# Performance work log

Measured on AMD Instinct MI355X. Metric: run time of the kernel, lower is better.

The kernel has to match this reference:

```python
import jax, jax.numpy as jnp
import numpy as np

CS = 128            # config.chunk_size
K = 8               # config.k + 1
EPS = 1e-6          # config.eps
L = K * CS          # extended_len = 1024


def setup_inputs() -> dict:
    key = jax.random.key(0)
    k1, k2 = jax.random.split(key)
    B, T, E = 2, 8192, 256
    x = jax.random.normal(k1, (B, T, E), dtype=jnp.float32)
    # xavier_normal_ on [CS, L]: std = sqrt(2 / (fan_in + fan_out))
    std = np.sqrt(2.0 / (CS + L)).astype(np.float32)
    down_proj = jax.random.normal(k2, (CS, L), dtype=jnp.float32) * std
    return {"x": x, "down_proj": down_proj}


def reference(x, down_proj):
    B, T, E = x.shape
    N = T // CS  # T chosen divisible by CS, so the pad branch is a no-op
    chunks = x.reshape(B, N, CS, E)

    # --- per-chunk retrieval scores (vectorized over the causal chunk loop) ---
    cn = chunks / (jnp.linalg.norm(chunks, axis=-1, keepdims=True) + EPS)
    # row-wise cosine sims between every pair of chunks: [B,N,N,CS,CS]
    sims = jnp.einsum('bice,bjde->bijcd', cn, cn)
    scores = sims.max(axis=-1).sum(axis=-1)              # [B,N,N]
    i_idx = jnp.arange(N)
    causal = i_idx[None, :] < i_idx[:, None]             # j < i allowed
    NEG = jnp.asarray(-1e9, x.dtype)
    scores = jnp.where(causal[None], scores, NEG)

    # --- topk selection, weights (num_sel_i = min(i, K-1)) ---
    vals, idx = jax.lax.top_k(scores, K - 1)             # descending, [B,N,K-1]
    num_sel = jnp.minimum(i_idx, K - 1)                  # [N]
    vmin_slot = jnp.clip(num_sel - 1, 0, K - 2)          # last valid slot = min of topk vals
    v_min = jnp.take_along_axis(vals, jnp.broadcast_to(vmin_slot[None, :, None], (B, N, 1)), axis=-1)
    slot = jnp.arange(K - 1)
    valid = slot[None, :] < num_sel[:, None]             # [N,K-1]
    w = jnp.where(valid[None], vals / (v_min + EPS), 0.0)  # [B,N,K-1]

    # --- weighted gather of selected chunks ---
    b_idx = jnp.arange(B)[:, None, None]
    sel = chunks[b_idx, idx]                             # [B,N,K-1,CS,E]
    weighted = sel * w[..., None, None]

    # --- left-pad to L: zeros occupy leftmost slots, then topk-ordered chunks, then cur ---
    shift = jnp.maximum(0, (K - 1) - i_idx)              # [N]
    src = jnp.clip(slot[None, :] - shift[:, None], 0, K - 2)   # [N,K-1]
    n_idx = jnp.arange(N)[None, :, None]
    arranged = weighted[b_idx, n_idx, src[None]]         # [B,N,K-1,CS,E]
    keep = slot[None, :] >= shift[:, None]
    arranged = jnp.where(keep[None, :, :, None, None], arranged, 0.0)

    ext = jnp.concatenate([arranged.reshape(B, N, (K - 1) * CS, E), chunks], axis=2)  # [B,N,L,E]
    # down_proj @ ext + x_chunks, then contract back to [B,T,E]
    out = jnp.einsum('cl,bnle->bnce', down_proj, ext) + chunks
    return out.reshape(B, N * CS, E)
```

## Files before the change

kernel.cpp:

```cpp
#include <hip/hip_runtime.h>
#include <hip/hip_bf16.h>

#define CS     128
#define EDIM   256
#define NBATCH 2
#define TLEN   8192
#define NCHUNK 64
#define LEXT   1024
#define KSEL   7

typedef __attribute__((ext_vector_type(8))) short   short8;
typedef __attribute__((ext_vector_type(4))) float   floatx4;

__device__ inline short bf16_of(float f) {
    __hip_bfloat16 h = __float2bfloat16(f);
    return *(short*)&h;
}
__device__ inline float f_of_bf16(short s) {
    __hip_bfloat16 h = *(__hip_bfloat16*)&s;
    return __bfloat162float(h);
}

__device__ inline void gl_lds16(const void* g, void* l) {
    __builtin_amdgcn_global_load_lds(
        (const __attribute__((address_space(1))) unsigned int*)g,
        (__attribute__((address_space(3))) unsigned int*)l, 16, 0, 0);
}

__global__ __launch_bounds__(256) void prep_kernel(const float* __restrict__ x,
                                                   const float* __restrict__ dp,
                                                   short* __restrict__ cn_hi,
                                                   short* __restrict__ cn_lo,
                                                   short* __restrict__ xt_hi,
                                                   short* __restrict__ dp_hi) {
    const int bx = blockIdx.x;
    if (bx >= 256) {
        int t = (bx - 256) * 256 + threadIdx.x;
#pragma unroll
        for (int u = 0; u < 16; ++u) {
            int idx = (t * 16 + u) * 4;
            float4 v = *(const float4*)(dp + idx);
            *(short4*)(dp_hi + idx) =
                make_short4(bf16_of(v.x), bf16_of(v.y), bf16_of(v.z), bf16_of(v.w));
        }
        return;
    }

    __shared__ float tile[64 * 257];
    const int b = bx >> 7, t0 = (bx & 127) * 64;
    const int tid = threadIdx.x;
    const int r = tid >> 2, q = tid & 3;

    const float* src = x + ((size_t)(b * TLEN + t0 + r)) * EDIM + q * 64;
    float* trow = &tile[r * 257 + q * 64];
    float s = 0.f;
#pragma unroll
    for (int u = 0; u < 16; ++u) {
        float4 v = *(const float4*)(src + u * 4);
        s += v.x * v.x + v.y * v.y + v.z * v.z + v.w * v.w;
        trow[u * 4 + 0] = v.x; trow[u * 4 + 1] = v.y;
        trow[u * 4 + 2] = v.z; trow[u * 4 + 3] = v.w;
    }
    s += __shfl_xor(s, 1);
    s += __shfl_xor(s, 2);
    const float rn = 1.0f / (sqrtf(s) + 1e-6f);

    short* ch = cn_hi + ((size_t)(b * TLEN + t0 + r)) * EDIM + q * 64;
    short* cl = cn_lo + ((size_t)(b * TLEN + t0 + r)) * EDIM + q * 64;
#pragma unroll
    for (int u = 0; u < 16; ++u) {
        short hs[4], ls[4];
#pragma unroll
        for (int k2 = 0; k2 < 4; ++k2) {
            float c = trow[u * 4 + k2] * rn;
            hs[k2] = bf16_of(c);
            ls[k2] = bf16_of(c - f_of_bf16(hs[k2]));
        }
        *(short4*)(ch + u * 4) = make_short4(hs[0], hs[1], hs[2], hs[3]);
        *(short4*)(cl + u * 4) = make_short4(ls[0], ls[1], ls[2], ls[3]);
    }
    __syncthreads();

    const int g16 = tid >> 4, tq = tid & 15;
#pragma unroll
    for (int it = 0; it < 16; ++it) {
        int e = g16 + it * 16;
        short hs2[4];
#pragma unroll
        for (int g = 0; g < 4; ++g)
            hs2[g] = bf16_of(tile[(tq * 4 + g) * 257 + e]);
        *(short4*)(xt_hi + ((size_t)(b * EDIM + e)) * TLEN + t0 + tq * 4)
            = make_short4(hs2[0], hs2[1], hs2[2], hs2[3]);
    }
}

__global__ __launch_bounds__(256) void scores_mfma(const short* __restrict__ cn_hi,
                                                   const short* __restrict__ cn_lo,
                                                   float* __restrict__ scores) {
    __shared__ short tiles[4][4096];
    double* red2  = (double*)&tiles[0][0];
    float*  redbuf = (float*)&tiles[0][8];

    const int p = blockIdx.x, b = blockIdx.y;
    int i = (int)((1.0f + sqrtf(1.0f + 8.0f * (float)p)) * 0.5f);
    while (i * (i - 1) / 2 > p) --i;
    while (i * (i + 1) / 2 <= p) ++i;
    const int j = p - i * (i - 1) / 2;

    const int tid  = threadIdx.x;
    const int w    = tid >> 6, lane = tid & 63;
    const int wr   = w >> 1, wc = w & 1;
    const int quad = lane >> 4, l15 = lane & 15;

    const short* sarr  = (w & 1) ? cn_lo : cn_hi;
    const size_t sbase = ((size_t)b * TLEN + ((w >> 1) ? j : i) * CS) * EDIM;
    const int rr  = lane >> 2;
    const int c16 = (lane & 3) * 8;
    const int csw = c16 ^ (((rr >> 1) & 3) * 8);
    const int q8  = (quad ^ ((l15 >> 1) & 3)) * 8;

    floatx4 acc[4][4];
#pragma unroll
    for (int rt = 0; rt < 4; ++rt)
#pragma unroll
        for (int ct = 0; ct < 4; ++ct) acc[rt][ct] = (floatx4){0.f, 0.f, 0.f, 0.f};

    for (int ks = 0; ks < 8; ++ks) {
        const short* gsrc = sarr + sbase + ks * 32 + csw;
        short* ldst = &tiles[w][0];
#pragma unroll
        for (int t = 0; t < 8; ++t)
            gl_lds16(gsrc + (size_t)(16 * t + rr) * EDIM, ldst + t * 512);
        __syncthreads();

        short8 bh[4], bl[4];
#pragma unroll
        for (int ct = 0; ct < 4; ++ct) {
            int r = wc * 64 + ct * 16 + l15;
            bh[ct] = *(const short8*)&tiles[2][r * 32 + q8];
            bl[ct] = *(const short8*)&tiles[3][r * 32 + q8];
        }
#pragma unroll
        for (int rt = 0; rt < 4; ++rt) {
            int r = wr * 64 + rt * 16 + l15;
            short8 ah = *(const short8*)&tiles[0][r * 32 + q8];
            short8 al = *(const short8*)&tiles[1][r * 32 + q8];
#pragma unroll
            for (int ct = 0; ct < 4; ++ct) {
                acc[rt][ct] = __builtin_amdgcn_mfma_f32_16x16x32_bf16(ah, bh[ct], acc[rt][ct], 0, 0, 0);
                acc[rt][ct] = __builtin_amdgcn_mfma_f32_16x16x32_bf16(ah, bl[ct], acc[rt][ct], 0, 0, 0);
                acc[rt][ct] = __builtin_amdgcn_mfma_f32_16x16x32_bf16(al, bh[ct], acc[rt][ct], 0, 0, 0);
            }
        }
        __syncthreads();
    }

#pragma unroll
    for (int rt = 0; rt < 4; ++rt) {
        float m[4];
#pragma unroll
        for (int reg = 0; reg < 4; ++reg) {
            float mm = acc[rt][0][reg];
#pragma unroll
            for (int ct = 1; ct < 4; ++ct) mm = fmaxf(mm, acc[rt][ct][reg]);
            m[reg] = mm;
        }
#pragma unroll
        for (int off = 1; off < 16; off <<= 1)
#pragma unroll
            for (int reg = 0; reg < 4; ++reg) m[reg] = fmaxf(m[reg], __shfl_xor(m[reg], off));
        if (l15 == 0) {
#pragma unroll
            for (int reg = 0; reg < 4; ++reg)
                redbuf[wc * 128 + wr * 64 + rt * 16 + quad * 4 + reg] = m[reg];
        }
    }
    __syncthreads();

    double part = 0.0;
    if (tid < 128) part = (double)fmaxf(redbuf[tid], redbuf[128 + tid]);
#pragma unroll
    for (int off = 1; off < 64; off <<= 1) part += __shfl_xor(part, off);
    if (lane == 0 && w < 2) red2[w] = part;
    __syncthreads();
    if (tid == 0) scores[(b * NCHUNK + i) * NCHUNK + j] = (float)(red2[0] + red2[1]);
}

__global__ __launch_bounds__(256) void out_mfma(const float* __restrict__ x,
                                                const short* __restrict__ dph,
                                                const short* __restrict__ xth,
                                                const float* __restrict__ scores,
                                                float* __restrict__ out) {
    __shared__ short As[2][128 * 32];
    __shared__ short Bs[2][64 * 32];
    __shared__ int   slist[8], sslot[8], snum;
    __shared__ float swei[8];

    const int eq = blockIdx.x, n = blockIdx.y, b = blockIdx.z;
    const int e0 = eq * 64;
    const int tid  = threadIdx.x;
    const int w    = tid >> 6, lane = tid & 63;
    const int wr   = w >> 1, wc = w & 1;
    const int quad = lane >> 4, l15 = lane & 15;
    const int rr   = lane >> 2;
    const int c16  = (lane & 3) * 8;
    const int csw  = c16 ^ (((rr >> 1) & 3) * 8);
    const int q8   = (quad ^ ((l15 >> 1) & 3)) * 8;

    if (w == 0) {
        const float* srow = scores + (b * NCHUNK + n) * NCHUNK;
        const int nsel = n < KSEL ? n : KSEL;
        float v = (lane < n) ? srow[lane] : -3.0e38f;
        float vals[KSEL];
        int   idxs[KSEL];
        for (int s2 = 0; s2 < nsel; ++s2) {
            float bv = v; int bi = lane;
#pragma unroll
            for (int off = 1; off < 64; off <<= 1) {
                float ov = __shfl_xor(bv, off);
                int   oi = __shfl_xor(bi, off);
                if (ov > bv || (ov == bv && oi < bi)) { bv = ov; bi = oi; }
            }
            vals[s2] = bv; idxs[s2] = bi;
            if (lane == bi) v = -3.0e38f;
        }
        if (lane == 0) {
            float vmin = (nsel > 0) ? vals[nsel - 1] : 0.0f;
            float inv  = 1.0f / (vmin + 1e-6f);
            int shift  = KSEL - nsel;
            int c = 0;
            for (int s2 = 0; s2 < 8; ++s2) {
                int jj; float ww;
                if (s2 < KSEL) {
                    int tt = s2 - shift;
                    if (tt >= 0) { jj = idxs[tt]; ww = vals[tt] * inv; }
                    else         { jj = -1;       ww = 0.0f; }
                } else { jj = n; ww = 1.0f; }
                if (jj >= 0) { slist[c] = jj; sslot[c] = s2; swei[c] = ww; ++c; }
            }
            snum = c;
        }
    }
    __syncthreads();
    const int NS = snum * 4;

    auto stage = [&](int st, int bf) {
        int sv = st >> 2, kk = st & 3;
        if (w < 2) {
            const short* gsrc = dph + (size_t)(sslot[sv] * 128 + kk * 32) + csw;
#pragma unroll
            for (int t = 0; t < 4; ++t)
                gl_lds16(gsrc + (size_t)(w * 64 + t * 16 + rr) * LEXT,
                         &As[bf][(w * 64 + t * 16) * 32]);
        } else {
            const short* gsrc = xth + ((size_t)(b * EDIM + e0)) * TLEN
                                + (size_t)(slist[sv] * CS + kk * 32) + csw;
#pragma unroll
            for (int t = 0; t < 2; ++t)
                gl_lds16(gsrc + (size_t)((w - 2) * 32 + t * 16 + rr) * TLEN,
                         &Bs[bf][((w - 2) * 32 + t * 16) * 32]);
        }
    };

    floatx4 accT[4][2], accP[4][2];
#pragma unroll
    for (int rt = 0; rt < 4; ++rt)
#pragma unroll
        for (int ct = 0; ct < 2; ++ct) accT[rt][ct] = (floatx4){0.f, 0.f, 0.f, 0.f};

    stage(0, 0);
    __syncthreads();

    int buf = 0;
    for (int st = 0; st < NS; ++st) {
        if (st + 1 < NS) stage(st + 1, buf ^ 1);

        if ((st & 3) == 0) {
#pragma unroll
            for (int rt = 0; rt < 4; ++rt)
#pragma unroll
                for (int ct = 0; ct < 2; ++ct) accP[rt][ct] = (floatx4){0.f, 0.f, 0.f, 0.f};
        }

        short8 bh[2];
#pragma unroll
        for (int ct = 0; ct < 2; ++ct) {
            int e = wc * 32 + ct * 16 + l15;
            bh[ct] = *(const short8*)&Bs[buf][e * 32 + q8];
        }
#pragma unroll
        for (int rt = 0; rt < 4; ++rt) {
            int r = wr * 64 + rt * 16 + l15;
            short8 ah = *(const short8*)&As[buf][r * 32 + q8];
#pragma unroll
            for (int ct = 0; ct < 2; ++ct)
                accP[rt][ct] = __builtin_amdgcn_mfma_f32_16x16x32_bf16(ah, bh[ct], accP[rt][ct], 0, 0, 0);
        }

        if ((st & 3) == 3) {
            float wcur = swei[st >> 2];
#pragma unroll
            for (int rt = 0; rt < 4; ++rt)
#pragma unroll
                for (int ct = 0; ct < 2; ++ct)
#pragma unroll
                    for (int reg = 0; reg < 4; ++reg)
                        accT[rt][ct][reg] += wcur * accP[rt][ct][reg];
        }
        __syncthreads();
        buf ^= 1;
    }

#pragma unroll
    for (int rt = 0; rt < 4; ++rt)
#pragma unroll
        for (int ct = 0; ct < 2; ++ct) {
#pragma unroll
            for (int reg = 0; reg < 4; ++reg) {
                int row = wr * 64 + rt * 16 + quad * 4 + reg;
                int col = wc * 32 + ct * 16 + l15;
                size_t o = ((size_t)(b * TLEN + n * CS + row)) * EDIM + e0 + col;
                out[o] = accT[rt][ct][reg] + x[o];
            }
        }
}

extern "C" void kernel_launch(void* const* d_in, const int* in_sizes, int n_in,
                              void* d_out, int out_size, void* d_ws, size_t ws_size,
                              hipStream_t stream) {
    const float* x  = (const float*)d_in[0];
    const float* dp = (const float*)d_in[1];
    float* out = (float*)d_out;

    char* ws = (char*)d_ws;
    short* cn_hi  = (short*)(ws);
    short* cn_lo  = (short*)(ws + (8u << 20));
    short* xt_hi  = (short*)(ws + (16u << 20));
    short* dp_hi  = (short*)(ws + (24u << 20));
    float* scores = (float*)(ws + (25u << 20));

    prep_kernel <<<dim3(264), 256, 0, stream>>>(x, dp, cn_hi, cn_lo, xt_hi, dp_hi);
    scores_mfma <<<dim3(NCHUNK * (NCHUNK - 1) / 2, NBATCH), 256, 0, stream>>>(cn_hi, cn_lo, scores);
    out_mfma    <<<dim3(4, NCHUNK, NBATCH), 256, 0, stream>>>(x, dp_hi, xt_hi, scores, out);
}
```

Before: 213.7 us.

## Double-buffer scores kernel and use partial vmcnt waits with raw barriers

The scores kernel now double-buffers its LDS tiles and prefetches the next k-slice before computing on the current one. Both the scores and projection kernels replace __syncthreads with a raw s_barrier preceded by a partial s_waitcnt vmcnt, so prefetch loads stay in flight across the barrier. MFMA sections are wrapped in s_setprio to favour matrix issue. The aim is to overlap global-to-LDS loads with MFMA work. The cost is double the LDS in the scores kernel, which may lower occupancy, and a risk of races if the hand-written vmcnt counts are wrong.

```diff
diff --git a/kernel.cpp b/kernel.cpp
--- a/kernel.cpp
+++ b/kernel.cpp
@@ -26,6 +26,8 @@
         (const __attribute__((address_space(1))) unsigned int*)g,
         (__attribute__((address_space(3))) unsigned int*)l, 16, 0, 0);
 }
+
+#define RAW_BAR() asm volatile("s_barrier" ::: "memory")
 
 __global__ __launch_bounds__(256) void prep_kernel(const float* __restrict__ x,
                                                    const float* __restrict__ dp,
@@ -97,9 +99,9 @@
 __global__ __launch_bounds__(256) void scores_mfma(const short* __restrict__ cn_hi,
                                                    const short* __restrict__ cn_lo,
                                                    float* __restrict__ scores) {
-    __shared__ short tiles[4][4096];
-    double* red2  = (double*)&tiles[0][0];
-    float*  redbuf = (float*)&tiles[0][8];
+    __shared__ short tiles[2][4][4096];
+    double* red2   = (double*)&tiles[0][0][0];
+    float*  redbuf = (float*)&tiles[0][0][8];
 
     const int p = blockIdx.x, b = blockIdx.y;
     int i = (int)((1.0f + sqrtf(1.0f + 8.0f * (float)p)) * 0.5f);
@@ -119,32 +121,44 @@
     const int csw = c16 ^ (((rr >> 1) & 3) * 8);
     const int q8  = (quad ^ ((l15 >> 1) & 3)) * 8;
 
-    floatx4 acc[4][4];
-#pragma unroll
-    for (int rt = 0; rt < 4; ++rt)
-#pragma unroll
-        for (int ct = 0; ct < 4; ++ct) acc[rt][ct] = (floatx4){0.f, 0.f, 0.f, 0.f};
-
-    for (int ks = 0; ks < 8; ++ks) {
+    auto stage = [&](int ks, int bf) {
         const short* gsrc = sarr + sbase + ks * 32 + csw;
-        short* ldst = &tiles[w][0];
+        short* ldst = &tiles[bf][w][0];
 #pragma unroll
         for (int t = 0; t < 8; ++t)
             gl_lds16(gsrc + (size_t)(16 * t + rr) * EDIM, ldst + t * 512);
-        __syncthreads();
+    };
+
+    floatx4 acc[4][4];
+#pragma unroll
+    for (int rt = 0; rt < 4; ++rt)
+#pragma unroll
+        for (int ct = 0; ct < 4; ++ct) acc[rt][ct] = (floatx4){0.f, 0.f, 0.f, 0.f};
+
+    stage(0, 0);
+    int buf = 0;
+    for (int ks = 0; ks < 8; ++ks) {
+        if (ks < 7) {
+            stage(ks + 1, buf ^ 1);
+            asm volatile("s_waitcnt vmcnt(8)" ::: "memory");
+        } else {
+            asm volatile("s_waitcnt vmcnt(0)" ::: "memory");
+        }
+        RAW_BAR();
 
         short8 bh[4], bl[4];
 #pragma unroll
         for (int ct = 0; ct < 4; ++ct) {
             int r = wc * 64 + ct * 16 + l15;
-            bh[ct] = *(const short8*)&tiles[2][r * 32 + q8];
-            bl[ct] = *(const short8*)&tiles[3][r * 32 + q8];
-        }
+            bh[ct] = *(const short8*)&tiles[buf][2][r * 32 + q8];
+            bl[ct] = *(const short8*)&tiles[buf][3][r * 32 + q8];
+        }
+        __builtin_amdgcn_s_setprio(1);
 #pragma unroll
         for (int rt = 0; rt < 4; ++rt) {
             int r = wr * 64 + rt * 16 + l15;
-            short8 ah = *(const short8*)&tiles[0][r * 32 + q8];
-            short8 al = *(const short8*)&tiles[1][r * 32 + q8];
+            short8 ah = *(const short8*)&tiles[buf][0][r * 32 + q8];
+            short8 al = *(const short8*)&tiles[buf][1][r * 32 + q8];
 #pragma unroll
             for (int ct = 0; ct < 4; ++ct) {
                 acc[rt][ct] = __builtin_amdgcn_mfma_f32_16x16x32_bf16(ah, bh[ct], acc[rt][ct], 0, 0, 0);
@@ -152,7 +166,9 @@
                 acc[rt][ct] = __builtin_amdgcn_mfma_f32_16x16x32_bf16(al, bh[ct], acc[rt][ct], 0, 0, 0);
             }
         }
-        __syncthreads();
+        __builtin_amdgcn_s_setprio(0);
+        RAW_BAR();
+        buf ^= 1;
     }
 
 #pragma unroll
@@ -269,11 +285,16 @@
         for (int ct = 0; ct < 2; ++ct) accT[rt][ct] = (floatx4){0.f, 0.f, 0.f, 0.f};
 
     stage(0, 0);
-    __syncthreads();
-
     int buf = 0;
     for (int st = 0; st < NS; ++st) {
-        if (st + 1 < NS) stage(st + 1, buf ^ 1);
+        if (st + 1 < NS) {
+            stage(st + 1, buf ^ 1);
+            if (w < 2) asm volatile("s_waitcnt vmcnt(4)" ::: "memory");
+            else       asm volatile("s_waitcnt vmcnt(2)" ::: "memory");
+        } else {
+            asm volatile("s_waitcnt vmcnt(0)" ::: "memory");
+        }
+        RAW_BAR();
 
         if ((st & 3) == 0) {
 #pragma unroll
@@ -288,6 +309,7 @@
             int e = wc * 32 + ct * 16 + l15;
             bh[ct] = *(const short8*)&Bs[buf][e * 32 + q8];
         }
+        __builtin_amdgcn_s_setprio(1);
 #pragma unroll
         for (int rt = 0; rt < 4; ++rt) {
             int r = wr * 64 + rt * 16 + l15;
@@ -296,6 +318,7 @@
             for (int ct = 0; ct < 2; ++ct)
                 accP[rt][ct] = __builtin_amdgcn_mfma_f32_16x16x32_bf16(ah, bh[ct], accP[rt][ct], 0, 0, 0);
         }
+        __builtin_amdgcn_s_setprio(0);
 
         if ((st & 3) == 3) {
             float wcur = swei[st >> 2];
@@ -307,7 +330,7 @@
                     for (int reg = 0; reg < 4; ++reg)
                         accT[rt][ct][reg] += wcur * accP[rt][ct][reg];
         }
-        __syncthreads();
+        RAW_BAR();
         buf ^= 1;
     }
 
```

Result: faster. 203.2 us (-4.9%).
